# Kernel tuning notes

Hardware: AMD Instinct MI355X
Metric: run time of the kernel (lower is better)

The kernel has to match this reference:

```python
import jax, jax.numpy as jnp
import numpy as np

L, B, E, H = 1024, 8, 512, 8
D = E // H
THRESH = 0.1  # sparsity_threshold
W_STD = 0.1   # keeps logits spread so threshold mask is non-trivial


def setup_inputs() -> dict:
    k0 = jax.random.key(0)
    ks = jax.random.split(k0, 7)
    return {
        "query": jax.random.normal(ks[0], (L, B, E), jnp.float32),
        "key": jax.random.normal(ks[1], (L, B, E), jnp.float32),
        "value": jax.random.normal(ks[2], (L, B, E), jnp.float32),
        "Wq": jax.random.normal(ks[3], (E, E), jnp.float32) * W_STD,
        "bq": jnp.zeros((E,), jnp.float32),
        "Wk": jax.random.normal(ks[4], (E, E), jnp.float32) * W_STD,
        "bk": jnp.zeros((E,), jnp.float32),
    }


def reference(query, key, value, Wq, bq, Wk, bk):
    # query/key/value: (L, B, E), seq-first as in nn.MultiheadAttention
    Lq, Bq, Eq = query.shape
    S = key.shape[0]
    q = (query @ Wq.T + bq).reshape(Lq, Bq, H, D)
    k = (key @ Wk.T + bk).reshape(S, Bq, H, D)
    scale = 1.0 / jnp.sqrt(jnp.asarray(D, q.dtype))
    scores = jnp.einsum('lbhd,sbhd->bhls', q, k) * scale  # [B,H,L,S]
    attn = jax.nn.softmax(scores, axis=-1)
    attn_avg = attn.mean(axis=1)  # averaged over heads -> [B,L,S]
    # threshold-mask + renormalize
    sw = jnp.where(attn_avg > THRESH, attn_avg, jnp.zeros((), attn_avg.dtype))
    sw = sw / (sw.sum(axis=-1, keepdims=True) + 1e-6)
    # second matmul against the RAW value tensor: [B,L,S] @ [B,S,E] -> [L,B,E]
    out = jnp.einsum('bls,sbe->lbe', sw, value)
    return out, sw
```

## Files before the change

kernel.cpp:

```cpp
#include <hip/hip_runtime.h>


#define THRESH 0.1f
#define PLANE (8 * 8 * 1024 * 64)

typedef __attribute__((ext_vector_type(8))) short bf8_t;
typedef __attribute__((ext_vector_type(4))) float f4_t;

#define MFMA16(a, b, c) __builtin_amdgcn_mfma_f32_16x16x32_bf16(a, b, c, 0, 0, 0)

__device__ __forceinline__ unsigned short f2bf(float x) {
  unsigned int u = __float_as_uint(x);
  u += 0x7FFFu + ((u >> 16) & 1u);
  return (unsigned short)(u >> 16);
}
__device__ __forceinline__ float bf2f(unsigned short h) {
  return __uint_as_float(((unsigned int)h) << 16);
}

__global__ __launch_bounds__(256) void proj_kernel(
    const float* __restrict__ A,
    const float* __restrict__ W,
    const float* __restrict__ bias,
    unsigned short* __restrict__ outp)
{
  __shared__ float As[16][132];
  __shared__ float Ws[16][132];
  const int t  = threadIdx.x;
  const int bm = blockIdx.x;
  const int bn = blockIdx.y;
  const int ty = t >> 4;
  const int tx = t & 15;
  const int lr  = t >> 2;
  const int lc4 = (t & 3) << 2;

  const float* Arow0 = A + (size_t)(bm * 128 + lr) * 512 + lc4;
  const float* Arow1 = Arow0 + 64 * 512;
  const float* Wrow0 = W + (size_t)(bn * 128 + lr) * 512 + lc4;
  const float* Wrow1 = Wrow0 + 64 * 512;

  float acc[8][8] = {};

  for (int k0 = 0; k0 < 512; k0 += 16) {
    float4 a0 = *(const float4*)(Arow0 + k0);
    float4 a1 = *(const float4*)(Arow1 + k0);
    float4 w0 = *(const float4*)(Wrow0 + k0);
    float4 w1 = *(const float4*)(Wrow1 + k0);
    __syncthreads();
    As[lc4 + 0][lr] = a0.x; As[lc4 + 1][lr] = a0.y; As[lc4 + 2][lr] = a0.z; As[lc4 + 3][lr] = a0.w;
    As[lc4 + 0][lr + 64] = a1.x; As[lc4 + 1][lr + 64] = a1.y; As[lc4 + 2][lr + 64] = a1.z; As[lc4 + 3][lr + 64] = a1.w;
    Ws[lc4 + 0][lr] = w0.x; Ws[lc4 + 1][lr] = w0.y; Ws[lc4 + 2][lr] = w0.z; Ws[lc4 + 3][lr] = w0.w;
    Ws[lc4 + 0][lr + 64] = w1.x; Ws[lc4 + 1][lr + 64] = w1.y; Ws[lc4 + 2][lr + 64] = w1.z; Ws[lc4 + 3][lr + 64] = w1.w;
    __syncthreads();
    #pragma unroll
    for (int kk = 0; kk < 16; ++kk) {
      float4 av0 = *(const float4*)&As[kk][ty * 8];
      float4 av1 = *(const float4*)&As[kk][ty * 8 + 4];
      float4 bv0 = *(const float4*)&Ws[kk][tx * 8];
      float4 bv1 = *(const float4*)&Ws[kk][tx * 8 + 4];
      float ar[8] = {av0.x, av0.y, av0.z, av0.w, av1.x, av1.y, av1.z, av1.w};
      float br[8] = {bv0.x, bv0.y, bv0.z, bv0.w, bv1.x, bv1.y, bv1.z, bv1.w};
      #pragma unroll
      for (int i = 0; i < 8; ++i)
        #pragma unroll
        for (int j = 0; j < 8; ++j)
          acc[i][j] += ar[i] * br[j];
    }
  }

  #pragma unroll
  for (int i = 0; i < 8; ++i) {
    const int gr = bm * 128 + ty * 8 + i;
    const int l = gr >> 3;
    const int b = gr & 7;
    #pragma unroll
    for (int jv = 0; jv < 8; jv += 4) {
      const int gc = bn * 128 + tx * 8 + jv;
      const int h = gc >> 6;
      const int d = gc & 63;
      const size_t off = ((size_t)((b * 8 + h) * 1024 + l)) * 64 + d;
      ushort4 ph, pm, pl;
      #pragma unroll
      for (int q = 0; q < 4; ++q) {
        float x = acc[i][jv + q] + bias[gc + q];
        unsigned short b1 = f2bf(x);  float r1 = x  - bf2f(b1);
        unsigned short b2 = f2bf(r1); float r2 = r1 - bf2f(b2);
        unsigned short b3 = f2bf(r2);
        ((unsigned short*)&ph)[q] = b1;
        ((unsigned short*)&pm)[q] = b2;
        ((unsigned short*)&pl)[q] = b3;
      }
      *(ushort4*)&outp[off] = ph;
      *(ushort4*)&outp[(size_t)PLANE + off] = pm;
      *(ushort4*)&outp[(size_t)2 * PLANE + off] = pl;
    }
  }
}

__global__ __launch_bounds__(512, 2) void attn_mfma_kernel(
    const unsigned short* __restrict__ qs,
    const unsigned short* __restrict__ ks,
    float* __restrict__ sw)
{
  const int bx = blockIdx.x;
  const int b  = bx & 7;
  const int l0 = (bx >> 3) << 5;
  const int tid  = threadIdx.x;
  const int w    = tid >> 6;
  const int lane = tid & 63;
  const int c    = lane & 15;
  const int g    = lane >> 4;

  __shared__ float red[8][32];
  __shared__ float redc[32];

  f4_t avg[2][8];
  #pragma unroll
  for (int rt = 0; rt < 2; ++rt)
    #pragma unroll
    for (int ct = 0; ct < 8; ++ct)
      avg[rt][ct] = (f4_t){0.f, 0.f, 0.f, 0.f};

  for (int h = 0; h < 8; ++h) {
    const size_t qbase = ((size_t)((b * 8 + h) * 1024 + l0)) * 64;
    const size_t kbase = ((size_t)((b * 8 + h) * 1024)) * 64;

    bf8_t qf[3][2][2];
    #pragma unroll
    for (int p = 0; p < 3; ++p)
      #pragma unroll
      for (int rt = 0; rt < 2; ++rt)
        #pragma unroll
        for (int kc = 0; kc < 2; ++kc)
          qf[p][rt][kc] = *(const bf8_t*)&qs[(size_t)p * PLANE + qbase +
                                             (size_t)(rt * 16 + c) * 64 + kc * 32 + g * 8];

    f4_t acc[2][8];
    #pragma unroll
    for (int rt = 0; rt < 2; ++rt)
      #pragma unroll
      for (int ct = 0; ct < 8; ++ct)
        acc[rt][ct] = (f4_t){0.f, 0.f, 0.f, 0.f};

    #pragma unroll
    for (int ct = 0; ct < 8; ++ct) {
      const size_t kb = kbase + (size_t)(w * 128 + ct * 16 + c) * 64 + g * 8;
      #pragma unroll
      for (int kc = 0; kc < 2; ++kc) {
        bf8_t kh = *(const bf8_t*)&ks[kb + kc * 32];
        bf8_t km = *(const bf8_t*)&ks[(size_t)PLANE + kb + kc * 32];
        bf8_t kl = *(const bf8_t*)&ks[(size_t)2 * PLANE + kb + kc * 32];
        #pragma unroll
        for (int rt = 0; rt < 2; ++rt) {
          acc[rt][ct] = MFMA16(qf[0][rt][kc], kh, acc[rt][ct]);
          acc[rt][ct] = MFMA16(qf[0][rt][kc], km, acc[rt][ct]);
          acc[rt][ct] = MFMA16(qf[1][rt][kc], kh, acc[rt][ct]);
          acc[rt][ct] = MFMA16(qf[0][rt][kc], kl, acc[rt][ct]);
          acc[rt][ct] = MFMA16(qf[1][rt][kc], km, acc[rt][ct]);
          acc[rt][ct] = MFMA16(qf[2][rt][kc], kh, acc[rt][ct]);
        }
      }
    }

    float mloc[2][4];
    #pragma unroll
    for (int rt = 0; rt < 2; ++rt)
      #pragma unroll
      for (int reg = 0; reg < 4; ++reg) {
        float m = acc[rt][0][reg];
        #pragma unroll
        for (int ct = 1; ct < 8; ++ct) m = fmaxf(m, acc[rt][ct][reg]);
        #pragma unroll
        for (int off = 8; off > 0; off >>= 1) m = fmaxf(m, __shfl_xor(m, off));
        mloc[rt][reg] = m;
      }
    if (c == 0) {
      #pragma unroll
      for (int rt = 0; rt < 2; ++rt)
        #pragma unroll
        for (int reg = 0; reg < 4; ++reg)
          red[w][rt * 16 + g * 4 + reg] = mloc[rt][reg];
    }
    __syncthreads();
    if (tid < 32) {
      float m = red[0][tid];
      #pragma unroll
      for (int w2 = 1; w2 < 8; ++w2) m = fmaxf(m, red[w2][tid]);
      redc[tid] = m;
    }
    __syncthreads();
    float mrow[2][4];
    #pragma unroll
    for (int rt = 0; rt < 2; ++rt)
      #pragma unroll
      for (int reg = 0; reg < 4; ++reg)
        mrow[rt][reg] = redc[rt * 16 + g * 4 + reg];

    float sloc[2][4] = {};
    #pragma unroll
    for (int rt = 0; rt < 2; ++rt)
      #pragma unroll
      for (int ct = 0; ct < 8; ++ct)
        #pragma unroll
        for (int reg = 0; reg < 4; ++reg) {
          float p = __expf(0.125f * (acc[rt][ct][reg] - mrow[rt][reg]));
          acc[rt][ct][reg] = p;
          sloc[rt][reg] += p;
        }
    #pragma unroll
    for (int rt = 0; rt < 2; ++rt)
      #pragma unroll
      for (int reg = 0; reg < 4; ++reg) {
        float s = sloc[rt][reg];
        #pragma unroll
        for (int off = 8; off > 0; off >>= 1) s += __shfl_xor(s, off);
        sloc[rt][reg] = s;
      }
    if (c == 0) {
      #pragma unroll
      for (int rt = 0; rt < 2; ++rt)
        #pragma unroll
        for (int reg = 0; reg < 4; ++reg)
          red[w][rt * 16 + g * 4 + reg] = sloc[rt][reg];
    }
    __syncthreads();
    if (tid < 32) {
      float s = red[0][tid];
      #pragma unroll
      for (int w2 = 1; w2 < 8; ++w2) s += red[w2][tid];
      redc[tid] = s;
    }
    __syncthreads();
    #pragma unroll
    for (int rt = 0; rt < 2; ++rt)
      #pragma unroll
      for (int reg = 0; reg < 4; ++reg) {
        const float inv = 0.125f / redc[rt * 16 + g * 4 + reg];
        #pragma unroll
        for (int ct = 0; ct < 8; ++ct)
          avg[rt][ct][reg] += acc[rt][ct][reg] * inv;
      }
  }

  float tl[2][4] = {};
  #pragma unroll
  for (int rt = 0; rt < 2; ++rt)
    #pragma unroll
    for (int ct = 0; ct < 8; ++ct)
      #pragma unroll
      for (int reg = 0; reg < 4; ++reg) {
        float v = avg[rt][ct][reg];
        v = v > THRESH ? v : 0.f;
        avg[rt][ct][reg] = v;
        tl[rt][reg] += v;
      }
  #pragma unroll
  for (int rt = 0; rt < 2; ++rt)
    #pragma unroll
    for (int reg = 0; reg < 4; ++reg) {
      float s = tl[rt][reg];
      #pragma unroll
      for (int off = 8; off > 0; off >>= 1) s += __shfl_xor(s, off);
      tl[rt][reg] = s;
    }
  if (c == 0) {
    #pragma unroll
    for (int rt = 0; rt < 2; ++rt)
      #pragma unroll
      for (int reg = 0; reg < 4; ++reg)
        red[w][rt * 16 + g * 4 + reg] = tl[rt][reg];
  }
  __syncthreads();
  if (tid < 32) {
    float s = red[0][tid];
    #pragma unroll
    for (int w2 = 1; w2 < 8; ++w2) s += red[w2][tid];
    redc[tid] = s;
  }
  __syncthreads();
  #pragma unroll
  for (int rt = 0; rt < 2; ++rt)
    #pragma unroll
    for (int reg = 0; reg < 4; ++reg) {
      const float inv = 1.f / (redc[rt * 16 + g * 4 + reg] + 1e-6f);
      const size_t rowoff = ((size_t)(b * 1024 + l0 + rt * 16 + g * 4 + reg)) * 1024;
      #pragma unroll
      for (int ct = 0; ct < 8; ++ct)
        sw[rowoff + w * 128 + ct * 16 + c] = avg[rt][ct][reg] * inv;
    }
}

__global__ __launch_bounds__(128) void pv_kernel(
    const float* __restrict__ sw,
    const float* __restrict__ value,
    float* __restrict__ out)
{
  const int l = blockIdx.x;
  const int b = blockIdx.y;
  const int t = threadIdx.x;
  __shared__ int cnt;
  __shared__ int   sidx[32];
  __shared__ float swt[32];
  if (t == 0) cnt = 0;
  __syncthreads();

  const float* row = sw + (size_t)(b * 1024 + l) * 1024;
  #pragma unroll
  for (int it = 0; it < 2; ++it) {
    const int s0 = (t + it * 128) * 4;
    float4 v = *(const float4*)(row + s0);
    if (v.x > 0.f) { int i = atomicAdd(&cnt, 1); if (i < 32) { sidx[i] = s0 + 0; swt[i] = v.x; } }
    if (v.y > 0.f) { int i = atomicAdd(&cnt, 1); if (i < 32) { sidx[i] = s0 + 1; swt[i] = v.y; } }
    if (v.z > 0.f) { int i = atomicAdd(&cnt, 1); if (i < 32) { sidx[i] = s0 + 2; swt[i] = v.z; } }
    if (v.w > 0.f) { int i = atomicAdd(&cnt, 1); if (i < 32) { sidx[i] = s0 + 3; swt[i] = v.w; } }
  }
  __syncthreads();
  const int n = cnt < 32 ? cnt : 32;

  const int e0 = t * 4;
  float4 o = {0.f, 0.f, 0.f, 0.f};
  for (int j = 0; j < n; ++j) {
    const float wgt = swt[j];
    const float4 vv = *(const float4*)(value + (size_t)(sidx[j] * 8 + b) * 512 + e0);
    o.x += wgt * vv.x; o.y += wgt * vv.y; o.z += wgt * vv.z; o.w += wgt * vv.w;
  }
  *(float4*)&out[(size_t)(l * 8 + b) * 512 + e0] = o;
}

extern "C" void kernel_launch(void* const* d_in, const int* in_sizes, int n_in,
                              void* d_out, int out_size, void* d_ws, size_t ws_size,
                              hipStream_t stream) {
  const float* query = (const float*)d_in[0];
  const float* key   = (const float*)d_in[1];
  const float* value = (const float*)d_in[2];
  const float* Wq    = (const float*)d_in[3];
  const float* bq    = (const float*)d_in[4];
  const float* Wk    = (const float*)d_in[5];
  const float* bk    = (const float*)d_in[6];

  float* out = (float*)d_out;
  float* sw  = out + (size_t)1024 * 8 * 512;

  unsigned short* qs = (unsigned short*)d_ws;
  unsigned short* ks = qs + (size_t)3 * PLANE;

  proj_kernel<<<dim3(64, 4), 256, 0, stream>>>(query, Wq, bq, qs);
  proj_kernel<<<dim3(64, 4), 256, 0, stream>>>(key,   Wk, bk, ks);
  attn_mfma_kernel<<<256, 512, 0, stream>>>(qs, ks, sw);
  pv_kernel<<<dim3(1024, 8), 128, 0, stream>>>(sw, value, out);
}
```

Baseline: 388.6 us.

## Merge Q/K projections into one launch, halve tiles, and prefetch loads

```diff
diff --git a/kernel.cpp b/kernel.cpp
--- a/kernel.cpp
+++ b/kernel.cpp
@@ -19,13 +19,19 @@
 }
 
 __global__ __launch_bounds__(256) void proj_kernel(
-    const float* __restrict__ A,
-    const float* __restrict__ W,
-    const float* __restrict__ bias,
-    unsigned short* __restrict__ outp)
+    const float* __restrict__ query, const float* __restrict__ key,
+    const float* __restrict__ Wq,    const float* __restrict__ Wk,
+    const float* __restrict__ bq,    const float* __restrict__ bk,
+    unsigned short* __restrict__ outq, unsigned short* __restrict__ outk)
 {
+  const int z = blockIdx.z;
+  const float* A    = z ? key : query;
+  const float* W    = z ? Wk  : Wq;
+  const float* bias = z ? bk  : bq;
+  unsigned short* outp = z ? outk : outq;
+
   __shared__ float As[16][132];
-  __shared__ float Ws[16][132];
+  __shared__ float Ws[16][68];
   const int t  = threadIdx.x;
   const int bm = blockIdx.x;
   const int bn = blockIdx.y;
@@ -36,64 +42,62 @@
 
   const float* Arow0 = A + (size_t)(bm * 128 + lr) * 512 + lc4;
   const float* Arow1 = Arow0 + 64 * 512;
-  const float* Wrow0 = W + (size_t)(bn * 128 + lr) * 512 + lc4;
-  const float* Wrow1 = Wrow0 + 64 * 512;
-
-  float acc[8][8] = {};
+  const float* Wrow  = W + (size_t)(bn * 64 + lr) * 512 + lc4;
+
+  float acc[8][4] = {};
+
+  float4 a0 = *(const float4*)(Arow0);
+  float4 a1 = *(const float4*)(Arow1);
+  float4 w0 = *(const float4*)(Wrow);
 
   for (int k0 = 0; k0 < 512; k0 += 16) {
-    float4 a0 = *(const float4*)(Arow0 + k0);
-    float4 a1 = *(const float4*)(Arow1 + k0);
-    float4 w0 = *(const float4*)(Wrow0 + k0);
-    float4 w1 = *(const float4*)(Wrow1 + k0);
     __syncthreads();
     As[lc4 + 0][lr] = a0.x; As[lc4 + 1][lr] = a0.y; As[lc4 + 2][lr] = a0.z; As[lc4 + 3][lr] = a0.w;
     As[lc4 + 0][lr + 64] = a1.x; As[lc4 + 1][lr + 64] = a1.y; As[lc4 + 2][lr + 64] = a1.z; As[lc4 + 3][lr + 64] = a1.w;
     Ws[lc4 + 0][lr] = w0.x; Ws[lc4 + 1][lr] = w0.y; Ws[lc4 + 2][lr] = w0.z; Ws[lc4 + 3][lr] = w0.w;
-    Ws[lc4 + 0][lr + 64] = w1.x; Ws[lc4 + 1][lr + 64] = w1.y; Ws[lc4 + 2][lr + 64] = w1.z; Ws[lc4 + 3][lr + 64] = w1.w;
-    __syncthreads();
+    __syncthreads();
+    if (k0 + 16 < 512) {
+      a0 = *(const float4*)(Arow0 + k0 + 16);
+      a1 = *(const float4*)(Arow1 + k0 + 16);
+      w0 = *(const float4*)(Wrow  + k0 + 16);
+    }
     #pragma unroll
     for (int kk = 0; kk < 16; ++kk) {
       float4 av0 = *(const float4*)&As[kk][ty * 8];
       float4 av1 = *(const float4*)&As[kk][ty * 8 + 4];
-      float4 bv0 = *(const float4*)&Ws[kk][tx * 8];
-      float4 bv1 = *(const float4*)&Ws[kk][tx * 8 + 4];
+      float4 bv0 = *(const float4*)&Ws[kk][tx * 4];
       float ar[8] = {av0.x, av0.y, av0.z, av0.w, av1.x, av1.y, av1.z, av1.w};
-      float br[8] = {bv0.x, bv0.y, bv0.z, bv0.w, bv1.x, bv1.y, bv1.z, bv1.w};
+      float br[4] = {bv0.x, bv0.y, bv0.z, bv0.w};
       #pragma unroll
       for (int i = 0; i < 8; ++i)
         #pragma unroll
-        for (int j = 0; j < 8; ++j)
+        for (int j = 0; j < 4; ++j)
           acc[i][j] += ar[i] * br[j];
     }
   }
 
+  const int h = bn;
   #pragma unroll
   for (int i = 0; i < 8; ++i) {
     const int gr = bm * 128 + ty * 8 + i;
     const int l = gr >> 3;
     const int b = gr & 7;
-    #pragma unroll
-    for (int jv = 0; jv < 8; jv += 4) {
-      const int gc = bn * 128 + tx * 8 + jv;
-      const int h = gc >> 6;
-      const int d = gc & 63;
-      const size_t off = ((size_t)((b * 8 + h) * 1024 + l)) * 64 + d;
-      ushort4 ph, pm, pl;
-      #pragma unroll
-      for (int q = 0; q < 4; ++q) {
-        float x = acc[i][jv + q] + bias[gc + q];
-        unsigned short b1 = f2bf(x);  float r1 = x  - bf2f(b1);
-        unsigned short b2 = f2bf(r1); float r2 = r1 - bf2f(b2);
-        unsigned short b3 = f2bf(r2);
-        ((unsigned short*)&ph)[q] = b1;
-        ((unsigned short*)&pm)[q] = b2;
-        ((unsigned short*)&pl)[q] = b3;
-      }
-      *(ushort4*)&outp[off] = ph;
-      *(ushort4*)&outp[(size_t)PLANE + off] = pm;
-      *(ushort4*)&outp[(size_t)2 * PLANE + off] = pl;
-    }
+    const int d = tx * 4;
+    const size_t off = ((size_t)((b * 8 + h) * 1024 + l)) * 64 + d;
+    ushort4 ph, pm, pl;
+    #pragma unroll
+    for (int q = 0; q < 4; ++q) {
+      float x = acc[i][q] + bias[h * 64 + d + q];
+      unsigned short b1 = f2bf(x);  float r1 = x  - bf2f(b1);
+      unsigned short b2 = f2bf(r1); float r2 = r1 - bf2f(b2);
+      unsigned short b3 = f2bf(r2);
+      ((unsigned short*)&ph)[q] = b1;
+      ((unsigned short*)&pm)[q] = b2;
+      ((unsigned short*)&pl)[q] = b3;
+    }
+    *(ushort4*)&outp[off] = ph;
+    *(ushort4*)&outp[(size_t)PLANE + off] = pm;
+    *(ushort4*)&outp[(size_t)2 * PLANE + off] = pl;
   }
 }
 
@@ -104,43 +108,35 @@
 {
   const int bx = blockIdx.x;
   const int b  = bx & 7;
-  const int l0 = (bx >> 3) << 5;
+  const int l0 = (bx >> 3) << 4;
   const int tid  = threadIdx.x;
   const int w    = tid >> 6;
   const int lane = tid & 63;
   const int c    = lane & 15;
   const int g    = lane >> 4;
 
-  __shared__ float red[8][32];
-  __shared__ float redc[32];
-
-  f4_t avg[2][8];
-  #pragma unroll
-  for (int rt = 0; rt < 2; ++rt)
-    #pragma unroll
-    for (int ct = 0; ct < 8; ++ct)
-      avg[rt][ct] = (f4_t){0.f, 0.f, 0.f, 0.f};
+  __shared__ float red[8][16];
+  __shared__ float redc[16];
+
+  f4_t avg[8];
+  #pragma unroll
+  for (int ct = 0; ct < 8; ++ct) avg[ct] = (f4_t){0.f, 0.f, 0.f, 0.f};
 
   for (int h = 0; h < 8; ++h) {
     const size_t qbase = ((size_t)((b * 8 + h) * 1024 + l0)) * 64;
     const size_t kbase = ((size_t)((b * 8 + h) * 1024)) * 64;
 
-    bf8_t qf[3][2][2];
+    bf8_t qf[3][2];
     #pragma unroll
     for (int p = 0; p < 3; ++p)
       #pragma unroll
-      for (int rt = 0; rt < 2; ++rt)
-        #pragma unroll
-        for (int kc = 0; kc < 2; ++kc)
-          qf[p][rt][kc] = *(const bf8_t*)&qs[(size_t)p * PLANE + qbase +
-                                             (size_t)(rt * 16 + c) * 64 + kc * 32 + g * 8];
-
-    f4_t acc[2][8];
-    #pragma unroll
-    for (int rt = 0; rt < 2; ++rt)
-      #pragma unroll
-      for (int ct = 0; ct < 8; ++ct)
-        acc[rt][ct] = (f4_t){0.f, 0.f, 0.f, 0.f};
+      for (int kc = 0; kc < 2; ++kc)
+        qf[p][kc] = *(const bf8_t*)&qs[(size_t)p * PLANE + qbase +
+                                       (size_t)c * 64 + kc * 32 + g * 8];
+
+    f4_t acc[8];
+    #pragma unroll
+    for (int ct = 0; ct < 8; ++ct) acc[ct] = (f4_t){0.f, 0.f, 0.f, 0.f};
 
     #pragma unroll
     for (int ct = 0; ct < 8; ++ct) {
@@ -150,81 +146,63 @@
         bf8_t kh = *(const bf8_t*)&ks[kb + kc * 32];
         bf8_t km = *(const bf8_t*)&ks[(size_t)PLANE + kb + kc * 32];
         bf8_t kl = *(const bf8_t*)&ks[(size_t)2 * PLANE + kb + kc * 32];
-        #pragma unroll
-        for (int rt = 0; rt < 2; ++rt) {
-          acc[rt][ct] = MFMA16(qf[0][rt][kc], kh, acc[rt][ct]);
-          acc[rt][ct] = MFMA16(qf[0][rt][kc], km, acc[rt][ct]);
-          acc[rt][ct] = MFMA16(qf[1][rt][kc], kh, acc[rt][ct]);
-          acc[rt][ct] = MFMA16(qf[0][rt][kc], kl, acc[rt][ct]);
-          acc[rt][ct] = MFMA16(qf[1][rt][kc], km, acc[rt][ct]);
-          acc[rt][ct] = MFMA16(qf[2][rt][kc], kh, acc[rt][ct]);
-        }
+        acc[ct] = MFMA16(qf[0][kc], kh, acc[ct]);
+        acc[ct] = MFMA16(qf[0][kc], km, acc[ct]);
+        acc[ct] = MFMA16(qf[1][kc], kh, acc[ct]);
+        acc[ct] = MFMA16(qf[0][kc], kl, acc[ct]);
+        acc[ct] = MFMA16(qf[1][kc], km, acc[ct]);
+        acc[ct] = MFMA16(qf[2][kc], kh, acc[ct]);
       }
     }
 
-    float mloc[2][4];
-    #pragma unroll
-    for (int rt = 0; rt < 2; ++rt)
-      #pragma unroll
-      for (int reg = 0; reg < 4; ++reg) {
-        float m = acc[rt][0][reg];
-        #pragma unroll
-        for (int ct = 1; ct < 8; ++ct) m = fmaxf(m, acc[rt][ct][reg]);
-        #pragma unroll
-        for (int off = 8; off > 0; off >>= 1) m = fmaxf(m, __shfl_xor(m, off));
-        mloc[rt][reg] = m;
-      }
+    float mloc[4];
+    #pragma unroll
+    for (int reg = 0; reg < 4; ++reg) {
+      float m = acc[0][reg];
+      #pragma unroll
+      for (int ct = 1; ct < 8; ++ct) m = fmaxf(m, acc[ct][reg]);
+      #pragma unroll
+      for (int off = 8; off > 0; off >>= 1) m = fmaxf(m, __shfl_xor(m, off));
+      mloc[reg] = m;
+    }
     if (c == 0) {
       #pragma unroll
-      for (int rt = 0; rt < 2; ++rt)
-        #pragma unroll
-        for (int reg = 0; reg < 4; ++reg)
-          red[w][rt * 16 + g * 4 + reg] = mloc[rt][reg];
-    }
-    __syncthreads();
-    if (tid < 32) {
+      for (int reg = 0; reg < 4; ++reg) red[w][g * 4 + reg] = mloc[reg];
+    }
+    __syncthreads();
+    if (tid < 16) {
       float m = red[0][tid];
       #pragma unroll
       for (int w2 = 1; w2 < 8; ++w2) m = fmaxf(m, red[w2][tid]);
       redc[tid] = m;
     }
     __syncthreads();
-    float mrow[2][4];
-    #pragma unroll
-    for (int rt = 0; rt < 2; ++rt)
-      #pragma unroll
-      for (int reg = 0; reg < 4; ++reg)
-        mrow[rt][reg] = redc[rt * 16 + g * 4 + reg];
-
-    float sloc[2][4] = {};
-    #pragma unroll
-    for (int rt = 0; rt < 2; ++rt)
-      #pragma unroll
-      for (int ct = 0; ct < 8; ++ct)
-        #pragma unroll
-        for (int reg = 0; reg < 4; ++reg) {
-          float p = __expf(0.125f * (acc[rt][ct][reg] - mrow[rt][reg]));
-          acc[rt][ct][reg] = p;
-          sloc[rt][reg] += p;
-        }
-    #pragma unroll
-    for (int rt = 0; rt < 2; ++rt)
+    float mrow[4];
+    #pragma unroll
+    for (int reg = 0; reg < 4; ++reg) mrow[reg] = redc[g * 4 + reg];
+
+    float sloc[4] = {};
+    #pragma unroll
+    for (int ct = 0; ct < 8; ++ct)
       #pragma unroll
       for (int reg = 0; reg < 4; ++reg) {
-        float s = sloc[rt][reg];
-        #pragma unroll
-        for (int off = 8; off > 0; off >>= 1) s += __shfl_xor(s, off);
-        sloc[rt][reg] = s;
+        float p = __expf(0.125f * (acc[ct][reg] - mrow[reg]));
+        acc[ct][reg] = p;
+        sloc[reg] += p;
       }
+    #pragma unroll
+    for (int reg = 0; reg < 4; ++reg) {
+      float s = sloc[reg];
+      #pragma unroll
+      for (int off = 8; off > 0; off >>= 1) s += __shfl_xor(s, off);
+      sloc[reg] = s;
+    }
     if (c == 0) {
       #pragma unroll
-      for (int rt = 0; rt < 2; ++rt)
-        #pragma unroll
-        for (int reg = 0; reg < 4; ++reg)
-          red[w][rt * 16 + g * 4 + reg] = sloc[rt][reg];
-    }
-    __syncthreads();
-    if (tid < 32) {
+      for (int reg = 0; reg < 4; ++reg) red[w][g * 4 + reg] = sloc[reg];
+    }
+    __syncthreads();
+    if (tid < 16) {
       float s = red[0][tid];
       #pragma unroll
       for (int w2 = 1; w2 < 8; ++w2) s += red[w2][tid];
@@ -232,46 +210,37 @@
     }
     __syncthreads();
     #pragma unroll
-    for (int rt = 0; rt < 2; ++rt)
-      #pragma unroll
-      for (int reg = 0; reg < 4; ++reg) {
-        const float inv = 0.125f / redc[rt * 16 + g * 4 + reg];
-        #pragma unroll
-        for (int ct = 0; ct < 8; ++ct)
-          avg[rt][ct][reg] += acc[rt][ct][reg] * inv;
-      }
-  }
-
-  float tl[2][4] = {};
-  #pragma unroll
-  for (int rt = 0; rt < 2; ++rt)
-    #pragma unroll
-    for (int ct = 0; ct < 8; ++ct)
-      #pragma unroll
-      for (int reg = 0; reg < 4; ++reg) {
-        float v = avg[rt][ct][reg];
-        v = v > THRESH ? v : 0.f;
-        avg[rt][ct][reg] = v;
-        tl[rt][reg] += v;
-      }
-  #pragma unroll
-  for (int rt = 0; rt < 2; ++rt)
-    #pragma unroll
     for (int reg = 0; reg < 4; ++reg) {
-      float s = tl[rt][reg];
-      #pragma unroll
-      for (int off = 8; off > 0; off >>= 1) s += __shfl_xor(s, off);
-      tl[rt][reg] = s;
-    }
+      const float inv = 0.125f / redc[g * 4 + reg];
+      #pragma unroll
+      for (int ct = 0; ct < 8; ++ct)
+        avg[ct][reg] += acc[ct][reg] * inv;
+    }
+  }
+
+  float tl[4] = {};
+  #pragma unroll
+  for (int ct = 0; ct < 8; ++ct)
+    #pragma unroll
+    for (int reg = 0; reg < 4; ++reg) {
+      float v = avg[ct][reg];
+      v = v > THRESH ? v : 0.f;
+      avg[ct][reg] = v;
+      tl[reg] += v;
+    }
+  #pragma unroll
+  for (int reg = 0; reg < 4; ++reg) {
+    float s = tl[reg];
+    #pragma unroll
+    for (int off = 8; off > 0; off >>= 1) s += __shfl_xor(s, off);
+    tl[reg] = s;
+  }
   if (c == 0) {
     #pragma unroll
-    for (int rt = 0; rt < 2; ++rt)
-      #pragma unroll
-      for (int reg = 0; reg < 4; ++reg)
-        red[w][rt * 16 + g * 4 + reg] = tl[rt][reg];
+    for (int reg = 0; reg < 4; ++reg) red[w][g * 4 + reg] = tl[reg];
   }
   __syncthreads();
-  if (tid < 32) {
+  if (tid < 16) {
     float s = red[0][tid];
     #pragma unroll
     for (int w2 = 1; w2 < 8; ++w2) s += red[w2][tid];
@@ -279,15 +248,13 @@
   }
   __syncthreads();
   #pragma unroll
-  for (int rt = 0; rt < 2; ++rt)
-    #pragma unroll
-    for (int reg = 0; reg < 4; ++reg) {
-      const float inv = 1.f / (redc[rt * 16 + g * 4 + reg] + 1e-6f);
-      const size_t rowoff = ((size_t)(b * 1024 + l0 + rt * 16 + g * 4 + reg)) * 1024;
-      #pragma unroll
-      for (int ct = 0; ct < 8; ++ct)
-        sw[rowoff + w * 128 + ct * 16 + c] = avg[rt][ct][reg] * inv;
-    }
+  for (int reg = 0; reg < 4; ++reg) {
+    const float inv = 1.f / (redc[g * 4 + reg] + 1e-6f);
+    const size_t rowoff = ((size_t)(b * 1024 + l0 + g * 4 + reg)) * 1024;
+    #pragma unroll
+    for (int ct = 0; ct < 8; ++ct)
+      sw[rowoff + w * 128 + ct * 16 + c] = avg[ct][reg] * inv;
+  }
 }
 
 __global__ __launch_bounds__(128) void pv_kernel(
@@ -344,8 +311,7 @@
   unsigned short* qs = (unsigned short*)d_ws;
   unsigned short* ks = qs + (size_t)3 * PLANE;
 
-  proj_kernel<<<dim3(64, 4), 256, 0, stream>>>(query, Wq, bq, qs);
-  proj_kernel<<<dim3(64, 4), 256, 0, stream>>>(key,   Wk, bk, ks);
-  attn_mfma_kernel<<<256, 512, 0, stream>>>(qs, ks, sw);
+  proj_kernel<<<dim3(64, 8, 2), 256, 0, stream>>>(query, key, Wq, Wk, bq, bk, qs, ks);
+  attn_mfma_kernel<<<512, 512, 0, stream>>>(qs, ks, sw);
   pv_kernel<<<dim3(1024, 8), 128, 0, stream>>>(sw, value, out);
 }
```

Measured after the change: 418.1 us. +7.6%, slower.
